# Kernel tuning notes

Measured on AMD Instinct MI355X. Metric: run time of the kernel, lower is better.

## Reference

```python
import jax, jax.numpy as jnp
import numpy as np

N = 50000
E = 800000
D = 128
NUM_GRAPHS = 64
NEG_SLOPE = 0.2


def _gat_conv(x, src, dst, W, a_src, a_dst, bias):
    """PyG GATConv with heads=1, concat=True. src/dst include self-loops."""
    h = x @ W                                  # [N, D_out]
    alpha_s = h @ a_src                        # [N]
    alpha_d = h @ a_dst                        # [N]
    e = alpha_s[src] + alpha_d[dst]            # [E_tot] edge scores
    e = jnp.where(e > 0, e, NEG_SLOPE * e)     # LeakyReLU(0.2)
    # numerically-stable softmax over incoming edges of each dst node
    m = jax.ops.segment_max(e, dst, num_segments=N)
    m = jnp.where(jnp.isfinite(m), m, 0.0)
    ex = jnp.exp(e - m[dst])
    s = jax.ops.segment_sum(ex, dst, num_segments=N)
    coef = ex / (s[dst] + 1e-16)               # [E_tot]
    msg = h[src] * coef[:, None]               # [E_tot, D_out] gathered messages
    out = jax.ops.segment_sum(msg, dst, num_segments=N)
    return out + bias


def setup_inputs() -> dict:
    key = jax.random.key(0)
    ks = jax.random.split(key, 12)
    x = jax.random.normal(ks[0], (N, D), dtype=jnp.float32)
    edge_index = jax.random.randint(ks[1], (2, E), 0, N, dtype=jnp.int64)
    batch = jnp.sort(jax.random.randint(ks[2], (N,), 0, NUM_GRAPHS, dtype=jnp.int64))
    g = 1.0 / np.sqrt(D)
    W1 = jax.random.normal(ks[3], (D, D), dtype=jnp.float32) * g
    as1 = jax.random.normal(ks[4], (D,), dtype=jnp.float32) * g
    ad1 = jax.random.normal(ks[5], (D,), dtype=jnp.float32) * g
    b1 = jnp.zeros((D,), dtype=jnp.float32)
    W2 = jax.random.normal(ks[6], (D, D), dtype=jnp.float32) * g
    as2 = jax.random.normal(ks[7], (D,), dtype=jnp.float32) * g
    ad2 = jax.random.normal(ks[8], (D,), dtype=jnp.float32) * g
    b2 = jnp.zeros((D,), dtype=jnp.float32)
    return {"x": x, "edge_index": edge_index, "batch": batch,
            "W1": W1, "as1": as1, "ad1": ad1, "b1": b1,
            "W2": W2, "as2": as2, "ad2": ad2, "b2": b2}


def reference(x, edge_index, batch, W1, as1, ad1, b1, W2, as2, ad2, b2):
    # PyG GATConv adds self-loops by default
    loops = jnp.arange(N, dtype=edge_index.dtype)
    src = jnp.concatenate([edge_index[0], loops])
    dst = jnp.concatenate([edge_index[1], loops])
    feats = _gat_conv(x, src, dst, W1, as1, ad1, b1)
    feats = _gat_conv(feats, src, dst, W2, as2, ad2, b2)
    # global mean pool over graphs in the batch
    sums = jax.ops.segment_sum(feats, batch, num_segments=NUM_GRAPHS)
    counts = jax.ops.segment_sum(jnp.ones((N,), feats.dtype), batch, num_segments=NUM_GRAPHS)
    pooled = sums / jnp.maximum(counts, 1.0)[:, None]
    return feats, pooled
```

## Files before the change

kernel.cpp:

```cpp
#include <hip/hip_runtime.h>

#define NN 50000
#define NE 800000
#define DIM 128
#define NG 64
#define ETOT (NE + NN)
#define NEG_SLOPE 0.2f
#define PB 200
#define MAXLG 8
#define NSH 8
#define SHW ((NN + NSH - 1) / NSH)
#define NB_SCAN ((NN + 255) / 256)

typedef unsigned int uint32;
typedef unsigned short ushort;
typedef short bf16x8 __attribute__((ext_vector_type(8)));
typedef float f32x4 __attribute__((ext_vector_type(4)));

static __device__ __forceinline__ uint32 f2bf_pack(float lo, float hi) {
  uint32 a = __float_as_uint(lo), b = __float_as_uint(hi);
  a = (a + 0x7fffu + ((a >> 16) & 1u)) >> 16;
  b = (b + 0x7fffu + ((b >> 16) & 1u)) >> 16;
  return a | (b << 16);
}
static __device__ __forceinline__ ushort f2bf1(float x) {
  uint32 a = __float_as_uint(x);
  a = (a + 0x7fffu + ((a >> 16) & 1u)) >> 16;
  return (ushort)a;
}
static __device__ __forceinline__ float bf_lo(uint32 u) { return __uint_as_float(u << 16); }
static __device__ __forceinline__ float bf_hi(uint32 u) { return __uint_as_float(u & 0xffff0000u); }


__global__ __launch_bounds__(256) void k_init(const float* __restrict__ W1, const float* __restrict__ W2,
                                              ushort* __restrict__ wt1, ushort* __restrict__ wt2,
                                              int* deg, int* fill, float* pooled, float* cnt) {
  int i = blockIdx.x * 256 + threadIdx.x;
  if (i < NN) { deg[i] = 1; fill[i] = 1; }
  if (i < NG * DIM) pooled[i] = 0.f;
  if (i < NG) cnt[i] = 0.f;
  if (i < DIM * DIM) {
    int n = i >> 7, k = i & 127;
    wt1[i] = f2bf1(W1[k * DIM + n]);
    wt2[i] = f2bf1(W2[k * DIM + n]);
  }
}

__global__ __launch_bounds__(256) void k_count(const int* __restrict__ dst, int* __restrict__ deg) {
  int e = blockIdx.x * 256 + threadIdx.x;
  if (e < NE) atomicAdd(&deg[dst[e]], 1);
}


__global__ __launch_bounds__(256) void k_scan1(const int* __restrict__ deg, int* __restrict__ offs,
                                               int* __restrict__ bsum) {
  __shared__ int ws[4];
  const int i = blockIdx.x * 256 + threadIdx.x;
  const int lane = threadIdx.x & 63, wid = threadIdx.x >> 6;
  int x = (i < NN) ? deg[i] : 0;
#pragma unroll
  for (int off = 1; off < 64; off <<= 1) {
    int t = __shfl_up(x, off, 64);
    if (lane >= off) x += t;
  }
  if (lane == 63) ws[wid] = x;
  __syncthreads();
  int pre = 0;
#pragma unroll
  for (int j = 0; j < 3; ++j) if (j < wid) pre += ws[j];
  x += pre;
  if (i < NN) offs[i + 1] = x;
  if (threadIdx.x == 255) bsum[blockIdx.x] = x;
}

__global__ __launch_bounds__(256) void k_scan2(const int* __restrict__ bsum, int* __restrict__ bpre) {
  __shared__ int ws[4];
  const int b = threadIdx.x;
  const int lane = b & 63, wid = b >> 6;
  int v = (b < NB_SCAN) ? bsum[b] : 0;
  int x = v;
#pragma unroll
  for (int off = 1; off < 64; off <<= 1) {
    int t = __shfl_up(x, off, 64);
    if (lane >= off) x += t;
  }
  if (lane == 63) ws[wid] = x;
  __syncthreads();
  int pre = 0;
#pragma unroll
  for (int j = 0; j < 3; ++j) if (j < wid) pre += ws[j];
  x += pre;
  if (b < NB_SCAN) bpre[b] = x - v;
}

__global__ __launch_bounds__(256) void k_scan3(int* __restrict__ offs, const int* __restrict__ bpre,
                                               const int* __restrict__ deg, int* __restrict__ csr) {
  const int i = blockIdx.x * 256 + threadIdx.x;
  if (i < NN) {
    int v = offs[i + 1] + bpre[blockIdx.x];
    offs[i + 1] = v;
    csr[v - deg[i]] = i;
  }
  if (i == 0) offs[0] = 0;
}

__global__ __launch_bounds__(256) void k_scatter(const int* __restrict__ src, const int* __restrict__ dst,
                                                 const int* __restrict__ offs, int* __restrict__ fill,
                                                 int* __restrict__ csr) {
  const int r = blockIdx.x & (NSH - 1);
  const int bi = blockIdx.x >> 3;
  const int nb = gridDim.x >> 3;
  const int lo = r * SHW, hi = min(lo + SHW, NN);
  for (int e = bi * 256 + threadIdx.x; e < NE; e += nb * 256) {
    int d = dst[e];
    if (d >= lo && d < hi) {
      int p = offs[d] + atomicAdd(&fill[d], 1);
      csr[p] = src[e];
    }
  }
}


template <int A16>
__global__ __launch_bounds__(256) void k_mm(const void* __restrict__ Xv, const ushort* __restrict__ WT,
                                            const float* __restrict__ a_s, const float* __restrict__ a_d,
                                            uint32* __restrict__ H16,
                                            float* __restrict__ alpha_s, float* __restrict__ alpha_d, int n) {
  __shared__ __align__(16) ushort sWT[DIM * DIM];
  __shared__ __align__(16) ushort sA[64 * DIM];
  const int tid = threadIdx.x;
  const int row0 = blockIdx.x * 64;

  {
    const int nr = tid >> 1, h2 = tid & 1;
    const uint4* wp = (const uint4*)(WT + nr * DIM + h2 * 64);
#pragma unroll
    for (int i = 0; i < 8; ++i) {
      uint4 v = wp[i];
      int byte = nr * 256 + (((h2 * 128 + i * 16)) ^ ((nr & 7) << 4));
      *(uint4*)((char*)sWT + byte) = v;
    }
  }
  {
    const int r = tid >> 2, q = tid & 3;
    int rg = row0 + r; if (rg > n - 1) rg = n - 1;
    if (A16) {
      const uint4* xp = (const uint4*)((const uint32*)Xv + (size_t)rg * 64 + q * 16);
#pragma unroll
      for (int i = 0; i < 4; ++i) {
        uint4 pk = xp[i];
        int byte = r * 256 + ((q * 64 + i * 16) ^ ((r & 7) << 4));
        *(uint4*)((char*)sA + byte) = pk;
      }
    } else {
      const float4* xp = (const float4*)((const float*)Xv + (size_t)rg * DIM + q * 32);
#pragma unroll
      for (int i = 0; i < 4; ++i) {
        float4 v0 = xp[2 * i], v1 = xp[2 * i + 1];
        uint4 pk = make_uint4(f2bf_pack(v0.x, v0.y), f2bf_pack(v0.z, v0.w),
                              f2bf_pack(v1.x, v1.y), f2bf_pack(v1.z, v1.w));
        int byte = r * 256 + ((q * 64 + i * 16) ^ ((r & 7) << 4));
        *(uint4*)((char*)sA + byte) = pk;
      }
    }
  }
  __syncthreads();

  const int l = tid & 63, wv = tid >> 6;
  const int jr = l & 15, g = l >> 4;
  const int m0 = wv * 16;
  f32x4 acc[8];
#pragma unroll
  for (int nt = 0; nt < 8; ++nt) acc[nt] = (f32x4){0.f, 0.f, 0.f, 0.f};

  const int ra = m0 + jr;
  const int abase = ra * 256, aswz = (ra & 7) << 4;
  const int bswz = (jr & 7) << 4;
#pragma unroll
  for (int kk = 0; kk < 4; ++kk) {
    const int kb = kk * 64 + g * 16;
    bf16x8 af = *(const bf16x8*)((const char*)sA + abase + (kb ^ aswz));
#pragma unroll
    for (int nt = 0; nt < 8; ++nt) {
      bf16x8 bfg = *(const bf16x8*)((const char*)sWT + (nt * 16 + jr) * 256 + (kb ^ bswz));
      acc[nt] = __builtin_amdgcn_mfma_f32_16x16x32_bf16(af, bfg, acc[nt], 0, 0, 0);
    }
  }

  float asv[8], adv[8];
#pragma unroll
  for (int nt = 0; nt < 8; ++nt) { asv[nt] = a_s[nt * 16 + jr]; adv[nt] = a_d[nt * 16 + jr]; }
#pragma unroll
  for (int j = 0; j < 4; ++j) {
    float ps = 0.f, pd = 0.f;
#pragma unroll
    for (int nt = 0; nt < 8; ++nt) {
      ps = fmaf(acc[nt][j], asv[nt], ps);
      pd = fmaf(acc[nt][j], adv[nt], pd);
    }
#pragma unroll
    for (int off = 1; off < 16; off <<= 1) {
      ps += __shfl_xor(ps, off, 64);
      pd += __shfl_xor(pd, off, 64);
    }
    int r = row0 + m0 + g * 4 + j;
    if (jr == 0 && r < n) { alpha_s[r] = ps; alpha_d[r] = pd; }
  }

  ushort* sOut = sA;
#pragma unroll
  for (int nt = 0; nt < 8; ++nt)
#pragma unroll
    for (int j = 0; j < 4; ++j)
      sOut[(m0 + g * 4 + j) * DIM + nt * 16 + jr] = f2bf1(acc[nt][j]);
#pragma unroll
  for (int i = 0; i < 4; ++i) {
    int r = row0 + m0 + (l >> 4) + i * 4;
    uint4 v = *(const uint4*)((const char*)sOut + m0 * 256 + l * 16 + i * 1024);
    if (r < n) *(uint4*)(H16 + (size_t)(row0 + m0) * 64 + l * 4 + i * 256) = v;
  }
}


#define GATHER4(J)                                                          \
  { int s0 = __shfl(sv, g32 + (J), 64), s1 = __shfl(sv, g32 + (J) + 1, 64), \
        s2 = __shfl(sv, g32 + (J) + 2, 64), s3 = __shfl(sv, g32 + (J) + 3, 64); \
    float c0 = __shfl(ex, g32 + (J), 64), c1 = __shfl(ex, g32 + (J) + 1, 64), \
          c2 = __shfl(ex, g32 + (J) + 2, 64), c3 = __shfl(ex, g32 + (J) + 3, 64); \
    uint32 v0 = H16[(size_t)s0 * 64 + u0];                                  \
    uint32 v1 = H16[(size_t)s1 * 64 + u0];                                  \
    uint32 v2 = H16[(size_t)s2 * 64 + u0];                                  \
    uint32 v3 = H16[(size_t)s3 * 64 + u0];                                  \
    ax = fmaf(c0, bf_lo(v0), ax); ay = fmaf(c0, bf_hi(v0), ay);             \
    ax = fmaf(c1, bf_lo(v1), ax); ay = fmaf(c1, bf_hi(v1), ay);             \
    ax = fmaf(c2, bf_lo(v2), ax); ay = fmaf(c2, bf_hi(v2), ay);             \
    ax = fmaf(c3, bf_lo(v3), ax); ay = fmaf(c3, bf_hi(v3), ay); }

#define GATHER1(J)                                                          \
  { int s0 = __shfl(sv, g32 + (J), 64); float c0 = __shfl(ex, g32 + (J), 64); \
    uint32 v0 = H16[(size_t)s0 * 64 + u0];                                  \
    ax = fmaf(c0, bf_lo(v0), ax); ay = fmaf(c0, bf_hi(v0), ay); }

template <int STORE16>
__global__ __launch_bounds__(256) void k_sm_aggr2(const int* __restrict__ offs, const int* __restrict__ csr,
                                                  const float* __restrict__ alpha_s, const float* __restrict__ alpha_d,
                                                  const uint32* __restrict__ H16, const float* __restrict__ bias,
                                                  float* __restrict__ out, uint32* __restrict__ out16) {
  const int b = blockIdx.x;
  const int half = b & 1;
  const int l = threadIdx.x & 63;
  const int sl = l & 31, g = l >> 5, g32 = g * 32;
  const int pair = (b >> 1) * 4 + (threadIdx.x >> 6);
  const int node = pair * 2 + g;
  const int bg = offs[node], eg = offs[node + 1];
  const int dg = eg - bg;
  const float ad = alpha_d[node];
  const int u0 = half * 32 + sl;

  const int maxd = max(dg, __shfl_xor(dg, 32, 64));
  float ax = 0.f, ay = 0.f, ssum = 0.f;

  if (maxd <= 32) {
    int sv = 0; float sc = -1e30f;
    if (sl < dg) {
      sv = csr[bg + sl];
      sc = alpha_s[sv] + ad;
      sc = sc > 0.f ? sc : NEG_SLOPE * sc;
    }
    float m = sc;
#pragma unroll
    for (int off = 1; off < 32; off <<= 1) m = fmaxf(m, __shfl_xor(m, off, 64));
    float ex = (sl < dg) ? __expf(sc - m) : 0.f;
    ssum = ex;
    int j = 0;
    for (; j + 7 < maxd; j += 8) { GATHER4(j); GATHER4(j + 4); }
    for (; j + 3 < maxd; j += 4) GATHER4(j);
    for (; j < maxd; ++j) GATHER1(j);
  } else {
    float m = -1e30f;
    for (int j = sl; j < dg; j += 32) {
      float sc = alpha_s[csr[bg + j]] + ad;
      sc = sc > 0.f ? sc : NEG_SLOPE * sc;
      m = fmaxf(m, sc);
    }
#pragma unroll
    for (int off = 1; off < 32; off <<= 1) m = fmaxf(m, __shfl_xor(m, off, 64));
    const int nch = (maxd + 31) >> 5;
    for (int c = 0; c < nch; ++c) {
      int j = c * 32 + sl;
      int sv = 0; float ex = 0.f;
      if (j < dg) {
        sv = csr[bg + j];
        float sc = alpha_s[sv] + ad;
        sc = sc > 0.f ? sc : NEG_SLOPE * sc;
        ex = __expf(sc - m);
      }
      ssum += ex;
      int cnt = min(32, maxd - c * 32);
      int jj = 0;
      for (; jj + 3 < cnt; jj += 4) GATHER4(jj);
      for (; jj < cnt; ++jj) GATHER1(jj);
    }
  }

#pragma unroll
  for (int off = 1; off < 32; off <<= 1) ssum += __shfl_xor(ssum, off, 64);
  const float inv = 1.f / (ssum + 1e-16f);
  const float2 bb = *(const float2*)(bias + 2 * u0);
  const float ox = ax * inv + bb.x, oy = ay * inv + bb.y;
  if (STORE16) {
    out16[(size_t)node * 64 + u0] = f2bf_pack(ox, oy);
  } else {
    *(float2*)(out + (size_t)node * DIM + 2 * u0) = make_float2(ox, oy);
  }
}


__global__ __launch_bounds__(256) void k_pool_partial(const float* __restrict__ feats,
                                                      const int* __restrict__ batch,
                                                      float* __restrict__ pooled, float* __restrict__ cnt) {
  __shared__ float acc[4][MAXLG][DIM];
  __shared__ float lcnt[4][MAXLG];
  const int tid = threadIdx.x;
  const int wid = tid >> 6, l = tid & 63;
  for (int i = tid; i < 4 * MAXLG * DIM; i += 256) ((float*)acc)[i] = 0.f;
  if (tid < 4 * MAXLG) ((float*)lcnt)[tid] = 0.f;
  __syncthreads();

  const int chunk = (NN + PB - 1) / PB;
  const int beg = blockIdx.x * chunk;
  const int end = min(beg + chunk, NN);
  const int g0 = (beg < NN) ? batch[beg] : 0;

  for (int node = beg + wid; node < end; node += 4) {
    int lg = batch[node] - g0;
    float2 v = *(const float2*)(feats + (size_t)node * DIM + 2 * l);
    if (lg < MAXLG) {
      acc[wid][lg][2 * l] += v.x;
      acc[wid][lg][2 * l + 1] += v.y;
      if (l == 0) lcnt[wid][lg] += 1.f;
    } else {
      atomicAdd(&pooled[(g0 + lg) * DIM + 2 * l], v.x);
      atomicAdd(&pooled[(g0 + lg) * DIM + 2 * l + 1], v.y);
      if (l == 0) atomicAdd(&cnt[g0 + lg], 1.f);
    }
  }
  __syncthreads();

  for (int i = tid; i < MAXLG * DIM; i += 256) {
    int lg = i >> 7, d = i & (DIM - 1);
    float s = acc[0][lg][d] + acc[1][lg][d] + acc[2][lg][d] + acc[3][lg][d];
    if (s != 0.f) atomicAdd(&pooled[(g0 + lg) * DIM + d], s);
  }
  if (tid < MAXLG) {
    float s = lcnt[0][tid] + lcnt[1][tid] + lcnt[2][tid] + lcnt[3][tid];
    if (s != 0.f) atomicAdd(&cnt[g0 + tid], s);
  }
}

__global__ __launch_bounds__(256) void k_pool_norm(float* pooled, const float* __restrict__ cnt) {
  int i = blockIdx.x * 256 + threadIdx.x;
  if (i < NG * DIM) pooled[i] /= fmaxf(cnt[i >> 7], 1.f);
}


static inline size_t pad256(size_t x) { return (x + 255) & ~(size_t)255; }

extern "C" void kernel_launch(void* const* d_in, const int* in_sizes, int n_in,
                              void* d_out, int out_size, void* d_ws, size_t ws_size,
                              hipStream_t stream) {
  const float* x   = (const float*)d_in[0];
  const int* ei    = (const int*)d_in[1];
  const int* batch = (const int*)d_in[2];
  const float* W1  = (const float*)d_in[3];
  const float* as1 = (const float*)d_in[4];
  const float* ad1 = (const float*)d_in[5];
  const float* b1  = (const float*)d_in[6];
  const float* W2  = (const float*)d_in[7];
  const float* as2 = (const float*)d_in[8];
  const float* ad2 = (const float*)d_in[9];
  const float* b2  = (const float*)d_in[10];

  float* out_feats = (float*)d_out;
  float* pooled    = out_feats + (size_t)NN * DIM;

  const int* src = ei;
  const int* dst = ei + NE;

  char* w = (char*)d_ws;
  uint32* h16 = (uint32*)w;   w += pad256((size_t)NN * 64 * 4);
  uint32* f116 = (uint32*)w;  w += pad256((size_t)NN * 64 * 4);
  float* alpha_s = (float*)w; w += pad256((size_t)NN * 4);
  float* alpha_d = (float*)w; w += pad256((size_t)NN * 4);
  int* deg  = (int*)w;        w += pad256((size_t)NN * 4);
  int* offs = (int*)w;        w += pad256((size_t)(NN + 1) * 4);
  int* fill = (int*)w;        w += pad256((size_t)NN * 4);
  int* csr  = (int*)w;        w += pad256((size_t)ETOT * 4);
  float* cnt  = (float*)w;    w += pad256((size_t)NG * 4);
  int* bsum = (int*)w;        w += pad256((size_t)NB_SCAN * 4);
  int* bpre = (int*)w;        w += pad256((size_t)NB_SCAN * 4);
  ushort* wt1 = (ushort*)w;   w += pad256((size_t)DIM * DIM * 2);
  ushort* wt2 = (ushort*)w;   w += pad256((size_t)DIM * DIM * 2);

  const int NB_N = (NN + 255) / 256;
  const int NB_E = (NE + 255) / 256;
  const int NB_A = (NN / 2 / 4) * 2;
  const int NB_G = (NN + 63) / 64;
  const int NB_SC = 1024;

  k_init<<<NB_N, 256, 0, stream>>>(W1, W2, wt1, wt2, deg, fill, pooled, cnt);
  k_count<<<NB_E, 256, 0, stream>>>(dst, deg);
  k_scan1<<<NB_SCAN, 256, 0, stream>>>(deg, offs, bsum);
  k_scan2<<<1, 256, 0, stream>>>(bsum, bpre);
  k_scan3<<<NB_SCAN, 256, 0, stream>>>(offs, bpre, deg, csr);
  k_scatter<<<NB_SC, 256, 0, stream>>>(src, dst, offs, fill, csr);

  k_mm<0><<<NB_G, 256, 0, stream>>>(x, wt1, as1, ad1, h16, alpha_s, alpha_d, NN);
  k_sm_aggr2<1><<<NB_A, 256, 0, stream>>>(offs, csr, alpha_s, alpha_d, h16, b1, nullptr, f116);

  k_mm<1><<<NB_G, 256, 0, stream>>>(f116, wt2, as2, ad2, h16, alpha_s, alpha_d, NN);
  k_sm_aggr2<0><<<NB_A, 256, 0, stream>>>(offs, csr, alpha_s, alpha_d, h16, b2, out_feats, nullptr);

  k_pool_partial<<<PB, 256, 0, stream>>>(out_feats, batch, pooled, cnt);
  k_pool_norm<<<(NG * DIM + 255) / 256, 256, 0, stream>>>(pooled, cnt);
}
```

Measured before the change: 213.6 us.

## Merge half-row blocks so each lane gathers 4 features via 8-byte loads

The aggregation kernel previously split each node's 128 features across two blocks, each handling 64 features with 4-byte loads. Now a single block handles the full row: each lane loads 8 bytes (4 bf16 features) per neighbor and keeps four accumulators, with vectorized bias reads and output stores. This halves the grid and removes the duplicated softmax/score work and the duplicated csr/alpha_s reads across the two halves. In exchange, each neighbor row is fetched in one wider request, and the unroll depth drops from 8 to 4 edges per iteration, which may reduce memory-level parallelism.

```diff
diff --git a/kernel.cpp b/kernel.cpp
--- a/kernel.cpp
+++ b/kernel.cpp
@@ -222,43 +222,38 @@
 }
 
 
-#define GATHER4(J)                                                          \
-  { int s0 = __shfl(sv, g32 + (J), 64), s1 = __shfl(sv, g32 + (J) + 1, 64), \
-        s2 = __shfl(sv, g32 + (J) + 2, 64), s3 = __shfl(sv, g32 + (J) + 3, 64); \
-    float c0 = __shfl(ex, g32 + (J), 64), c1 = __shfl(ex, g32 + (J) + 1, 64), \
-          c2 = __shfl(ex, g32 + (J) + 2, 64), c3 = __shfl(ex, g32 + (J) + 3, 64); \
-    uint32 v0 = H16[(size_t)s0 * 64 + u0];                                  \
-    uint32 v1 = H16[(size_t)s1 * 64 + u0];                                  \
-    uint32 v2 = H16[(size_t)s2 * 64 + u0];                                  \
-    uint32 v3 = H16[(size_t)s3 * 64 + u0];                                  \
-    ax = fmaf(c0, bf_lo(v0), ax); ay = fmaf(c0, bf_hi(v0), ay);             \
-    ax = fmaf(c1, bf_lo(v1), ax); ay = fmaf(c1, bf_hi(v1), ay);             \
-    ax = fmaf(c2, bf_lo(v2), ax); ay = fmaf(c2, bf_hi(v2), ay);             \
-    ax = fmaf(c3, bf_lo(v3), ax); ay = fmaf(c3, bf_hi(v3), ay); }
+#define GATHER2(J)                                                          \
+  { int s0 = __shfl(sv, g32 + (J), 64), s1 = __shfl(sv, g32 + (J) + 1, 64); \
+    float c0 = __shfl(ex, g32 + (J), 64), c1 = __shfl(ex, g32 + (J) + 1, 64); \
+    uint2 v0 = *(const uint2*)(H16 + ((size_t)s0 << 6) + su);               \
+    uint2 v1 = *(const uint2*)(H16 + ((size_t)s1 << 6) + su);               \
+    a0 = fmaf(c0, bf_lo(v0.x), a0); a1 = fmaf(c0, bf_hi(v0.x), a1);         \
+    a2 = fmaf(c0, bf_lo(v0.y), a2); a3 = fmaf(c0, bf_hi(v0.y), a3);         \
+    a0 = fmaf(c1, bf_lo(v1.x), a0); a1 = fmaf(c1, bf_hi(v1.x), a1);         \
+    a2 = fmaf(c1, bf_lo(v1.y), a2); a3 = fmaf(c1, bf_hi(v1.y), a3); }
 
 #define GATHER1(J)                                                          \
   { int s0 = __shfl(sv, g32 + (J), 64); float c0 = __shfl(ex, g32 + (J), 64); \
-    uint32 v0 = H16[(size_t)s0 * 64 + u0];                                  \
-    ax = fmaf(c0, bf_lo(v0), ax); ay = fmaf(c0, bf_hi(v0), ay); }
+    uint2 v0 = *(const uint2*)(H16 + ((size_t)s0 << 6) + su);               \
+    a0 = fmaf(c0, bf_lo(v0.x), a0); a1 = fmaf(c0, bf_hi(v0.x), a1);         \
+    a2 = fmaf(c0, bf_lo(v0.y), a2); a3 = fmaf(c0, bf_hi(v0.y), a3); }
 
 template <int STORE16>
-__global__ __launch_bounds__(256) void k_sm_aggr2(const int* __restrict__ offs, const int* __restrict__ csr,
+__global__ __launch_bounds__(256) void k_sm_aggr3(const int* __restrict__ offs, const int* __restrict__ csr,
                                                   const float* __restrict__ alpha_s, const float* __restrict__ alpha_d,
                                                   const uint32* __restrict__ H16, const float* __restrict__ bias,
                                                   float* __restrict__ out, uint32* __restrict__ out16) {
-  const int b = blockIdx.x;
-  const int half = b & 1;
   const int l = threadIdx.x & 63;
   const int sl = l & 31, g = l >> 5, g32 = g * 32;
-  const int pair = (b >> 1) * 4 + (threadIdx.x >> 6);
+  const int su = sl * 2;
+  const int pair = blockIdx.x * 4 + (threadIdx.x >> 6);
   const int node = pair * 2 + g;
   const int bg = offs[node], eg = offs[node + 1];
   const int dg = eg - bg;
   const float ad = alpha_d[node];
-  const int u0 = half * 32 + sl;
 
   const int maxd = max(dg, __shfl_xor(dg, 32, 64));
-  float ax = 0.f, ay = 0.f, ssum = 0.f;
+  float a0 = 0.f, a1 = 0.f, a2 = 0.f, a3 = 0.f, ssum = 0.f;
 
   if (maxd <= 32) {
     int sv = 0; float sc = -1e30f;
@@ -273,8 +268,8 @@
     float ex = (sl < dg) ? __expf(sc - m) : 0.f;
     ssum = ex;
     int j = 0;
-    for (; j + 7 < maxd; j += 8) { GATHER4(j); GATHER4(j + 4); }
-    for (; j + 3 < maxd; j += 4) GATHER4(j);
+    for (; j + 3 < maxd; j += 4) { GATHER2(j); GATHER2(j + 2); }
+    for (; j + 1 < maxd; j += 2) GATHER2(j);
     for (; j < maxd; ++j) GATHER1(j);
   } else {
     float m = -1e30f;
@@ -298,7 +293,7 @@
       ssum += ex;
       int cnt = min(32, maxd - c * 32);
       int jj = 0;
-      for (; jj + 3 < cnt; jj += 4) GATHER4(jj);
+      for (; jj + 1 < cnt; jj += 2) GATHER2(jj);
       for (; jj < cnt; ++jj) GATHER1(jj);
     }
   }
@@ -306,12 +301,14 @@
 #pragma unroll
   for (int off = 1; off < 32; off <<= 1) ssum += __shfl_xor(ssum, off, 64);
   const float inv = 1.f / (ssum + 1e-16f);
-  const float2 bb = *(const float2*)(bias + 2 * u0);
-  const float ox = ax * inv + bb.x, oy = ay * inv + bb.y;
+  const float4 bb = *(const float4*)(bias + 4 * sl);
+  const float o0 = a0 * inv + bb.x, o1 = a1 * inv + bb.y;
+  const float o2 = a2 * inv + bb.z, o3 = a3 * inv + bb.w;
   if (STORE16) {
-    out16[(size_t)node * 64 + u0] = f2bf_pack(ox, oy);
+    uint2 pv = make_uint2(f2bf_pack(o0, o1), f2bf_pack(o2, o3));
+    *(uint2*)(out16 + (size_t)node * 64 + su) = pv;
   } else {
-    *(float2*)(out + (size_t)node * DIM + 2 * u0) = make_float2(ox, oy);
+    *(float4*)(out + (size_t)node * DIM + 4 * sl) = make_float4(o0, o1, o2, o3);
   }
 }
 
@@ -404,7 +401,7 @@
 
   const int NB_N = (NN + 255) / 256;
   const int NB_E = (NE + 255) / 256;
-  const int NB_A = (NN / 2 / 4) * 2;
+  const int NB_A = NN / 2 / 4;
   const int NB_G = (NN + 63) / 64;
   const int NB_SC = 1024;
 
@@ -416,10 +413,10 @@
   k_scatter<<<NB_SC, 256, 0, stream>>>(src, dst, offs, fill, csr);
 
   k_mm<0><<<NB_G, 256, 0, stream>>>(x, wt1, as1, ad1, h16, alpha_s, alpha_d, NN);
-  k_sm_aggr2<1><<<NB_A, 256, 0, stream>>>(offs, csr, alpha_s, alpha_d, h16, b1, nullptr, f116);
+  k_sm_aggr3<1><<<NB_A, 256, 0, stream>>>(offs, csr, alpha_s, alpha_d, h16, b1, nullptr, f116);
 
   k_mm<1><<<NB_G, 256, 0, stream>>>(f116, wt2, as2, ad2, h16, alpha_s, alpha_d, NN);
-  k_sm_aggr2<0><<<NB_A, 256, 0, stream>>>(offs, csr, alpha_s, alpha_d, h16, b2, out_feats, nullptr);
+  k_sm_aggr3<0><<<NB_A, 256, 0, stream>>>(offs, csr, alpha_s, alpha_d, h16, b2, out_feats, nullptr);
 
   k_pool_partial<<<PB, 256, 0, stream>>>(out_feats, batch, pooled, cnt);
   k_pool_norm<<<(NG * DIM + 255) / 256, 256, 0, stream>>>(pooled, cnt);
```

Result: no change. 209.9 us (-1.7%).
